# Optimization experiments

Hardware: AMD Instinct MI355X
Metric: run time of the kernel (lower is better)

The kernel has to match this reference:

```python
import jax, jax.numpy as jnp
import numpy as np

EPS = 1e-12
ALPHA = 100.0

def _l2norm(v, axis):
    n = jnp.sqrt(jnp.sum(v * v, axis=axis, keepdims=True))
    return v / jnp.maximum(n, EPS)

def setup_inputs() -> dict:
    key = jax.random.key(0)
    k1, k2, k3 = jax.random.split(key, 3)
    N, C, H, W, K = 64, 128, 64, 64, 64
    x = jax.random.normal(k1, (N, C, H, W), dtype=jnp.float32)
    xyz = jax.random.normal(k2, (N, 3, H * W), dtype=jnp.float32)
    centroids = jax.random.uniform(k3, (K, C), dtype=jnp.float32)
    # conv params are initialized from centroids as in _init_params
    conv_w = 2.0 * ALPHA * centroids              # [K, C] (1x1 kernel squeezed)
    conv_b = -ALPHA * jnp.linalg.norm(centroids, axis=1)  # [K]
    return {"x": x, "xyz": xyz, "centroids": centroids, "conv_w": conv_w, "conv_b": conv_b}

def reference(x, xyz, centroids, conv_w, conv_b):
    N, C = x.shape[:2]
    K = centroids.shape[0]
    # descriptor-wise L2 normalization over channel dim
    x = _l2norm(x, axis=1)
    xf = x.reshape(N, C, -1)                      # [N, C, P]
    # 1x1 conv == channel matmul; softmax over clusters
    logits = jnp.einsum('kc,ncp->nkp', conv_w, xf) + conv_b[None, :, None]
    a = jax.nn.softmax(logits, axis=1)            # [N, K, P]
    # vlad[n,k,c] = sum_p a*x  -  (sum_p a) * centroid  (algebraically equal to
    # the original broadcasted-residual construction, without the NKCP tensor)
    vlad = jnp.einsum('nkp,ncp->nkc', a, xf) - a.sum(axis=-1)[..., None] * centroids[None]
    vlad = _l2norm(vlad, axis=2)                  # intra-normalization
    vlad = vlad.reshape(N, -1)
    vlad = _l2norm(vlad, axis=1)
    return vlad[..., None]                        # [N, K*C, 1]
```

## Files before the change

kernel.cpp:

```cpp
#include <hip/hip_runtime.h>
#include <math.h>

#define N_ 64
#define C_ 128
#define K_ 64
#define P_ 4096
#define PT 32
#define TILES_PER_N 8
#define PB (P_ / TILES_PER_N)
#define NSUB (PB / PT)
#define XH_STR 132
#define XT_STR 36
#define AS_STR 66
#define RED_STR 33

typedef __attribute__((ext_vector_type(8))) short short8;
typedef __attribute__((ext_vector_type(4))) float f32x4;

union U4S8 { unsigned int u[4]; short8 s; };

__device__ __forceinline__ unsigned int pack_hl(float f) {
    unsigned int xb = __float_as_uint(f);
    float hif = __uint_as_float(xb & 0xffff0000u);
    float lo  = f - hif;
    unsigned int lob = __float_as_uint(lo) & 0xffff0000u;
    return (xb >> 16) | lob;
}

__device__ __forceinline__ void unpack8(const unsigned int p[8], short8& hi, short8& lo) {
    U4S8 h, l;
    #pragma unroll
    for (int j = 0; j < 4; ++j) {
        unsigned int a = p[2 * j], b = p[2 * j + 1];
        h.u[j] = (a & 0xffffu) | (b << 16);
        l.u[j] = (a >> 16) | (b & 0xffff0000u);
    }
    hi = h.s; lo = l.s;
}

#define MFMA16(a, b, c) __builtin_amdgcn_mfma_f32_16x16x32_bf16(a, b, c, 0, 0, 0)

__global__ __launch_bounds__(256, 3)
void netvlad_main(const float* __restrict__ x,
                  const float* __restrict__ conv_w,
                  const float* __restrict__ conv_b,
                  float* __restrict__ acc_part,
                  float* __restrict__ asum_part,
                  int use_atomic)
{
    __shared__ unsigned int xhat[PT * XH_STR];
    __shared__ unsigned int xT  [C_ * XT_STR];
    __shared__ unsigned int as_ [PT * AS_STR];
    __shared__ float        red [PT * RED_STR];
    __shared__ float        rn_ [PT];

    const int t  = threadIdx.x;
    const int wv = t >> 6;
    const int l  = t & 63;
    const int n    = blockIdx.x >> 3;
    const int tile = blockIdx.x & 7;

    const int mrow = l & 15;
    const int kq   = l >> 4;

    const int cq  = t >> 3;
    const int ppq = t & 7;

    const int scp   = 8 * wv + (l & 7);
    const int skseg = l >> 3;

    short8 whi[4], wlo[4];
    {
        const float* wrow = conv_w + (size_t)(16 * wv + mrow) * C_;
        #pragma unroll
        for (int s = 0; s < 4; ++s) {
            U4S8 h, lo_;
            #pragma unroll
            for (int j = 0; j < 4; ++j) {
                float f0 = wrow[s * 32 + kq * 8 + 2 * j];
                float f1 = wrow[s * 32 + kq * 8 + 2 * j + 1];
                unsigned int b0 = __float_as_uint(f0), b1 = __float_as_uint(f1);
                float l0 = f0 - __uint_as_float(b0 & 0xffff0000u);
                float l1 = f1 - __uint_as_float(b1 & 0xffff0000u);
                unsigned int lb0 = __float_as_uint(l0) >> 16;
                unsigned int lb1 = __float_as_uint(l1) >> 16;
                h.u[j]   = (b0 >> 16) | ((b1 >> 16) << 16);
                lo_.u[j] = lb0 | (lb1 << 16);
            }
            whi[s] = h.s; wlo[s] = lo_.s;
        }
    }

    float cb8[8];
    #pragma unroll
    for (int i = 0; i < 8; ++i) cb8[i] = conv_b[skseg * 8 + i];

    f32x4 accC[8];
    #pragma unroll
    for (int nt = 0; nt < 8; ++nt) accC[nt] = (f32x4){0.f, 0.f, 0.f, 0.f};
    float asum_acc[8];
    #pragma unroll
    for (int i = 0; i < 8; ++i) asum_acc[i] = 0.f;

    const float* xbase = x + ((size_t)n * C_) * P_ + tile * PB + 4 * ppq;

    float4 ld[4];
    #pragma unroll
    for (int cc = 0; cc < 4; ++cc)
        ld[cc] = *(const float4*)(xbase + (size_t)(4 * cq + cc) * P_);

    for (int sub = 0; sub < NSUB; ++sub) {
        __syncthreads();

        {
            unsigned int pk[4][4];
            float ssq[4] = {0.f, 0.f, 0.f, 0.f};
            #pragma unroll
            for (int cc = 0; cc < 4; ++cc) {
                const float* f = &ld[cc].x;
                #pragma unroll
                for (int j = 0; j < 4; ++j) {
                    pk[cc][j] = pack_hl(f[j]);
                    ssq[j] += f[j] * f[j];
                }
            }
            #pragma unroll
            for (int j = 0; j < 4; ++j) {
                uint4 v = make_uint4(pk[0][j], pk[1][j], pk[2][j], pk[3][j]);
                *(uint4*)(xhat + (4 * ppq + j) * XH_STR + 4 * cq) = v;
                red[(4 * ppq + j) * RED_STR + cq] = ssq[j];
            }
            #pragma unroll
            for (int cc = 0; cc < 4; ++cc) {
                uint4 v = make_uint4(pk[cc][0], pk[cc][1], pk[cc][2], pk[cc][3]);
                *(uint4*)(xT + (4 * cq + cc) * XT_STR + 4 * ppq) = v;
            }
        }
        if (sub + 1 < NSUB) {
            #pragma unroll
            for (int cc = 0; cc < 4; ++cc)
                ld[cc] = *(const float4*)(xbase + (size_t)(4 * cq + cc) * P_ + (sub + 1) * PT);
        }
        __syncthreads();

        if (t < PT) {
            float ss = 0.f;
            #pragma unroll
            for (int q = 0; q < 32; ++q) ss += red[t * RED_STR + q];
            rn_[t] = 1.f / fmaxf(sqrtf(ss), 1e-12f);
        }

        #pragma unroll
        for (int j = 0; j < 2; ++j) {
            f32x4 accA = (f32x4){0.f, 0.f, 0.f, 0.f};
            const unsigned int* rowp = xhat + (j * 16 + mrow) * XH_STR + kq * 8;
            #pragma unroll
            for (int s = 0; s < 4; ++s) {
                uint4 q0 = *(const uint4*)(rowp + s * 32);
                uint4 q1 = *(const uint4*)(rowp + s * 32 + 4);
                unsigned int p8[8] = {q0.x, q0.y, q0.z, q0.w, q1.x, q1.y, q1.z, q1.w};
                short8 bhi, blo;
                unpack8(p8, bhi, blo);
                accA = MFMA16(whi[s], bhi, accA);
                accA = MFMA16(whi[s], blo, accA);
                accA = MFMA16(wlo[s], bhi, accA);
                accA = MFMA16(wlo[s], blo, accA);
            }
            #pragma unroll
            for (int r = 0; r < 4; ++r)
                as_[(j * 16 + mrow) * AS_STR + 16 * wv + kq * 4 + r] =
                    __float_as_uint(accA[r]);
        }
        __syncthreads();

        {
            float rnv = rn_[scp];
            float lv[8];
            #pragma unroll
            for (int i = 0; i < 8; ++i)
                lv[i] = __uint_as_float(as_[scp * AS_STR + skseg * 8 + i]) * rnv + cb8[i];
            float m = lv[0];
            #pragma unroll
            for (int i = 1; i < 8; ++i) m = fmaxf(m, lv[i]);
            float s = 0.f;
            #pragma unroll
            for (int i = 0; i < 8; ++i) s += __expf(lv[i] - m);
            #pragma unroll
            for (int off = 8; off <= 32; off <<= 1) {
                float mo = __shfl_xor(m, off);
                float so = __shfl_xor(s, off);
                float Mn = fmaxf(m, mo);
                s = s * __expf(m - Mn) + so * __expf(mo - Mn);
                m = Mn;
            }
            float inv = 1.f / s;
            #pragma unroll
            for (int i = 0; i < 8; ++i) {
                float a = __expf(lv[i] - m) * inv;
                asum_acc[i] += a;
                as_[scp * AS_STR + skseg * 8 + i] = pack_hl(a * rnv);
            }
        }
        __syncthreads();

        {
            unsigned int pa[8];
            #pragma unroll
            for (int i = 0; i < 8; ++i)
                pa[i] = as_[(kq * 8 + i) * AS_STR + 16 * wv + mrow];
            short8 ahi, alo;
            unpack8(pa, ahi, alo);
            #pragma unroll
            for (int nt = 0; nt < 8; ++nt) {
                const unsigned int* rp = xT + (nt * 16 + mrow) * XT_STR + kq * 8;
                uint4 q0 = *(const uint4*)(rp);
                uint4 q1 = *(const uint4*)(rp + 4);
                unsigned int p8[8] = {q0.x, q0.y, q0.z, q0.w, q1.x, q1.y, q1.z, q1.w};
                short8 xhi, xlo;
                unpack8(p8, xhi, xlo);
                accC[nt] = MFMA16(ahi, xhi, accC[nt]);
                accC[nt] = MFMA16(ahi, xlo, accC[nt]);
                accC[nt] = MFMA16(alo, xhi, accC[nt]);
                accC[nt] = MFMA16(alo, xlo, accC[nt]);
            }
        }
    }

    __syncthreads();
    {
        #pragma unroll
        for (int i = 0; i < 8; ++i) {
            asum_acc[i] += __shfl_xor(asum_acc[i], 1);
            asum_acc[i] += __shfl_xor(asum_acc[i], 2);
            asum_acc[i] += __shfl_xor(asum_acc[i], 4);
        }
        float* fred = (float*)xhat;
        if ((l & 7) == 0) {
            #pragma unroll
            for (int i = 0; i < 8; ++i)
                fred[wv * 64 + skseg * 8 + i] = asum_acc[i];
        }
    }
    if (!use_atomic) {
        float* dst = acc_part + ((size_t)blockIdx.x * K_ + 16 * wv + kq * 4) * C_ + mrow;
        #pragma unroll
        for (int r = 0; r < 4; ++r)
            #pragma unroll
            for (int nt = 0; nt < 8; ++nt)
                dst[r * C_ + nt * 16] = accC[nt][r];
    } else {
        float* dst = acc_part + ((size_t)n * K_ + 16 * wv + kq * 4) * C_ + mrow;
        #pragma unroll
        for (int r = 0; r < 4; ++r)
            #pragma unroll
            for (int nt = 0; nt < 8; ++nt)
                atomicAdd(dst + r * C_ + nt * 16, accC[nt][r]);
    }
    __syncthreads();
    if (t < K_) {
        const float* fred = (const float*)xhat;
        float v = fred[0 * 64 + t] + fred[1 * 64 + t] + fred[2 * 64 + t] + fred[3 * 64 + t];
        if (use_atomic) atomicAdd(asum_part + n * K_ + t, v);
        else            asum_part[(size_t)blockIdx.x * K_ + t] = v;
    }
}

__global__ __launch_bounds__(256, 4)
void netvlad_finalize(const float* __restrict__ acc_part,
                      const float* __restrict__ asum_part,
                      const float* __restrict__ centroids,
                      float* __restrict__ out,
                      int npart)
{
    __shared__ float wred[4];
    const int t = threadIdx.x;
    const int n = blockIdx.x;
    const int k = t >> 2;
    const int part = t & 3;

    float a_k = 0.f;
    for (int s = 0; s < npart; ++s)
        a_k += asum_part[(size_t)(n * npart + s) * K_ + k];

    float4 vals[8];
    #pragma unroll
    for (int i = 0; i < 8; ++i) vals[i] = make_float4(0.f, 0.f, 0.f, 0.f);
    for (int s = 0; s < npart; ++s) {
        const float4* av = (const float4*)(acc_part
            + ((size_t)(n * npart + s) * K_ + k) * C_ + part * 32);
        #pragma unroll
        for (int i = 0; i < 8; ++i) {
            float4 a = av[i];
            vals[i].x += a.x; vals[i].y += a.y;
            vals[i].z += a.z; vals[i].w += a.w;
        }
    }

    const float4* cenv = (const float4*)(centroids + k * C_ + part * 32);
    float loc = 0.f;
    #pragma unroll
    for (int i = 0; i < 8; ++i) {
        float4 cv = cenv[i];
        float4 v = vals[i];
        v.x -= a_k * cv.x; v.y -= a_k * cv.y;
        v.z -= a_k * cv.z; v.w -= a_k * cv.w;
        vals[i] = v;
        loc += v.x * v.x + v.y * v.y + v.z * v.z + v.w * v.w;
    }
    loc += __shfl_xor(loc, 1);
    loc += __shfl_xor(loc, 2);
    float rk = 1.f / fmaxf(sqrtf(loc), 1e-12f);

    float tot = 0.f;
    #pragma unroll
    for (int i = 0; i < 8; ++i) {
        float4 v = vals[i];
        v.x *= rk; v.y *= rk; v.z *= rk; v.w *= rk;
        vals[i] = v;
        tot += v.x * v.x + v.y * v.y + v.z * v.z + v.w * v.w;
    }
    #pragma unroll
    for (int o = 1; o < 64; o <<= 1) tot += __shfl_xor(tot, o);
    if ((t & 63) == 0) wred[t >> 6] = tot;
    __syncthreads();
    float T = wred[0] + wred[1] + wred[2] + wred[3];
    float rtot = 1.f / fmaxf(sqrtf(T), 1e-12f);

    float4* outv = (float4*)(out + ((size_t)n * K_ + k) * C_ + part * 32);
    #pragma unroll
    for (int i = 0; i < 8; ++i) {
        float4 v = vals[i];
        v.x *= rtot; v.y *= rtot; v.z *= rtot; v.w *= rtot;
        outv[i] = v;
    }
}

extern "C" void kernel_launch(void* const* d_in, const int* in_sizes, int n_in,
                              void* d_out, int out_size, void* d_ws, size_t ws_size,
                              hipStream_t stream)
{
    const float* x      = (const float*)d_in[0];
    const float* cent   = (const float*)d_in[2];
    const float* conv_w = (const float*)d_in[3];
    const float* conv_b = (const float*)d_in[4];
    float* out = (float*)d_out;

    const int nblk = N_ * TILES_PER_N;
    size_t need = (size_t)nblk * K_ * C_ * sizeof(float)
                + (size_t)nblk * K_ * sizeof(float);
    int use_atomic = (ws_size >= need) ? 0 : 1;
    int npart = use_atomic ? 1 : TILES_PER_N;

    float* acc_part  = (float*)d_ws;
    float* asum_part = acc_part + (size_t)(use_atomic ? N_ : nblk) * K_ * C_;

    if (use_atomic) {
        size_t zbytes = ((size_t)N_ * K_ * C_ + (size_t)N_ * K_) * sizeof(float);
        hipMemsetAsync(d_ws, 0, zbytes, stream);
    }

    hipLaunchKernelGGL(netvlad_main, dim3(nblk), dim3(256), 0, stream,
                       x, conv_w, conv_b, acc_part, asum_part, use_atomic);
    hipLaunchKernelGGL(netvlad_finalize, dim3(N_), dim3(256), 0, stream,
                       acc_part, asum_part, cent, out, npart);
}
```

Before: 230.9 us.

## Split hi/lo bf16 planes in LDS with swizzle, drop lo*lo MFMA, retile waves

Stores x and the assignment matrix as separate pre-packed hi and lo bf16 planes in shared memory, using XOR-swizzled layouts, so MFMA operands load directly without unpack shuffles. The lo*lo MFMA term is dropped, leaving three MFMAs per product instead of four. The second GEMM is retiled so each wave owns 4x2 output tiles. The sum-of-squares reduction now uses cross-lane shuffles, and launch bounds drop to 2 blocks per SM. In exchange there is slightly lower precision, more LDS per block and possibly lower occupancy.

```diff
diff --git a/kernel.cpp b/kernel.cpp
--- a/kernel.cpp
+++ b/kernel.cpp
@@ -9,38 +9,24 @@
 #define TILES_PER_N 8
 #define PB (P_ / TILES_PER_N)
 #define NSUB (PB / PT)
-#define XH_STR 132
-#define XT_STR 36
-#define AS_STR 66
-#define RED_STR 33
 
 typedef __attribute__((ext_vector_type(8))) short short8;
 typedef __attribute__((ext_vector_type(4))) float f32x4;
 
-union U4S8 { unsigned int u[4]; short8 s; };
-
-__device__ __forceinline__ unsigned int pack_hl(float f) {
-    unsigned int xb = __float_as_uint(f);
-    float hif = __uint_as_float(xb & 0xffff0000u);
-    float lo  = f - hif;
-    unsigned int lob = __float_as_uint(lo) & 0xffff0000u;
-    return (xb >> 16) | lob;
-}
-
-__device__ __forceinline__ void unpack8(const unsigned int p[8], short8& hi, short8& lo) {
-    U4S8 h, l;
-    #pragma unroll
-    for (int j = 0; j < 4; ++j) {
-        unsigned int a = p[2 * j], b = p[2 * j + 1];
-        h.u[j] = (a & 0xffffu) | (b << 16);
-        l.u[j] = (a >> 16) | (b & 0xffff0000u);
-    }
-    hi = h.s; lo = l.s;
+union U4S8 { uint4 u4; unsigned int u[4]; short8 s; };
+
+__device__ __forceinline__ unsigned int pair_hi(float a, float b) {
+    return (__float_as_uint(b) & 0xffff0000u) | (__float_as_uint(a) >> 16);
+}
+__device__ __forceinline__ float lo_part(float f) {
+    return f - __uint_as_float(__float_as_uint(f) & 0xffff0000u);
 }
 
 #define MFMA16(a, b, c) __builtin_amdgcn_mfma_f32_16x16x32_bf16(a, b, c, 0, 0, 0)
 
-__global__ __launch_bounds__(256, 3)
+__device__ __forceinline__ int pmask(int p) { return (p & 7) ^ ((p >> 3) & 3); }
+
+__global__ __launch_bounds__(256, 2)
 void netvlad_main(const float* __restrict__ x,
                   const float* __restrict__ conv_w,
                   const float* __restrict__ conv_b,
@@ -48,10 +34,14 @@
                   float* __restrict__ asum_part,
                   int use_atomic)
 {
-    __shared__ unsigned int xhat[PT * XH_STR];
-    __shared__ unsigned int xT  [C_ * XT_STR];
-    __shared__ unsigned int as_ [PT * AS_STR];
-    __shared__ float        red [PT * RED_STR];
+    __shared__ unsigned int xhi [PT * 64];
+    __shared__ unsigned int xlo [PT * 64];
+    __shared__ unsigned int xthi[C_ * 20];
+    __shared__ unsigned int xtlo[C_ * 20];
+    __shared__ unsigned int ahi_[K_ * 20];
+    __shared__ unsigned int alo_[K_ * 20];
+    __shared__ float        asl [PT * 68];
+    __shared__ float        red2[4 * 33];
     __shared__ float        rn_ [PT];
 
     const int t  = threadIdx.x;
@@ -63,122 +53,140 @@
     const int mrow = l & 15;
     const int kq   = l >> 4;
 
+    const int ppq = t & 7;
     const int cq  = t >> 3;
-    const int ppq = t & 7;
-
-    const int scp   = 8 * wv + (l & 7);
-    const int skseg = l >> 3;
-
-    short8 whi[4], wlo[4];
-    {
-        const float* wrow = conv_w + (size_t)(16 * wv + mrow) * C_;
+
+    const int kseg = l >> 3;
+    const int scol = 8 * wv + (l & 7);
+
+    const int ntp = wv & 1;
+    const int mt0 = 2 * (wv >> 1);
+
+    short8 whi[2][4], wlo[2][4];
+    #pragma unroll
+    for (int mtl = 0; mtl < 2; ++mtl) {
+        const float* wr = conv_w + (size_t)((mt0 + mtl) * 16 + mrow) * C_;
         #pragma unroll
         for (int s = 0; s < 4; ++s) {
-            U4S8 h, lo_;
+            U4S8 h, lo;
             #pragma unroll
             for (int j = 0; j < 4; ++j) {
-                float f0 = wrow[s * 32 + kq * 8 + 2 * j];
-                float f1 = wrow[s * 32 + kq * 8 + 2 * j + 1];
-                unsigned int b0 = __float_as_uint(f0), b1 = __float_as_uint(f1);
-                float l0 = f0 - __uint_as_float(b0 & 0xffff0000u);
-                float l1 = f1 - __uint_as_float(b1 & 0xffff0000u);
-                unsigned int lb0 = __float_as_uint(l0) >> 16;
-                unsigned int lb1 = __float_as_uint(l1) >> 16;
-                h.u[j]   = (b0 >> 16) | ((b1 >> 16) << 16);
-                lo_.u[j] = lb0 | (lb1 << 16);
-            }
-            whi[s] = h.s; wlo[s] = lo_.s;
-        }
-    }
-
+                float f0 = wr[s * 32 + kq * 8 + 2 * j];
+                float f1 = wr[s * 32 + kq * 8 + 2 * j + 1];
+                h.u[j]  = pair_hi(f0, f1);
+                lo.u[j] = pair_hi(lo_part(f0), lo_part(f1));
+            }
+            whi[mtl][s] = h.s; wlo[mtl][s] = lo.s;
+        }
+    }
     float cb8[8];
     #pragma unroll
-    for (int i = 0; i < 8; ++i) cb8[i] = conv_b[skseg * 8 + i];
-
-    f32x4 accC[8];
-    #pragma unroll
-    for (int nt = 0; nt < 8; ++nt) accC[nt] = (f32x4){0.f, 0.f, 0.f, 0.f};
+    for (int i = 0; i < 8; ++i) cb8[i] = conv_b[kseg * 8 + i];
+
+    f32x4 accC[4][2];
+    #pragma unroll
+    for (int mt = 0; mt < 4; ++mt)
+        #pragma unroll
+        for (int ntl = 0; ntl < 2; ++ntl) accC[mt][ntl] = (f32x4){0.f, 0.f, 0.f, 0.f};
     float asum_acc[8];
     #pragma unroll
     for (int i = 0; i < 8; ++i) asum_acc[i] = 0.f;
 
-    const float* xbase = x + ((size_t)n * C_) * P_ + tile * PB + 4 * ppq;
+    const float* xb = x + ((size_t)n * C_) * P_ + tile * PB + 4 * ppq;
 
     float4 ld[4];
     #pragma unroll
     for (int cc = 0; cc < 4; ++cc)
-        ld[cc] = *(const float4*)(xbase + (size_t)(4 * cq + cc) * P_);
+        ld[cc] = *(const float4*)(xb + (size_t)(4 * cq + cc) * P_);
 
     for (int sub = 0; sub < NSUB; ++sub) {
         __syncthreads();
 
         {
-            unsigned int pk[4][4];
-            float ssq[4] = {0.f, 0.f, 0.f, 0.f};
+            const float* lf = (const float*)ld;
             #pragma unroll
             for (int cc = 0; cc < 4; ++cc) {
-                const float* f = &ld[cc].x;
+                float4 v = ld[cc];
+                int c = 4 * cq + cc;
+                uint2 wh; wh.x = pair_hi(v.x, v.y); wh.y = pair_hi(v.z, v.w);
+                *(uint2*)(xthi + c * 20 + 2 * ppq) = wh;
+                uint2 wl; wl.x = pair_hi(lo_part(v.x), lo_part(v.y));
+                wl.y = pair_hi(lo_part(v.z), lo_part(v.w));
+                *(uint2*)(xtlo + c * 20 + 2 * ppq) = wl;
+            }
+            float ssq[4];
+            #pragma unroll
+            for (int j = 0; j < 4; ++j) {
+                int p = 4 * ppq + j;
+                int ch = cq >> 1;
+                int chp = (ch & 8) | ((ch ^ pmask(p)) & 7);
+                int base = p * 64 + (chp << 2) + ((cq & 1) << 1);
+                float f0 = lf[0 * 4 + j], f1 = lf[1 * 4 + j];
+                float f2 = lf[2 * 4 + j], f3 = lf[3 * 4 + j];
+                uint2 wh; wh.x = pair_hi(f0, f1); wh.y = pair_hi(f2, f3);
+                *(uint2*)(xhi + base) = wh;
+                uint2 wl; wl.x = pair_hi(lo_part(f0), lo_part(f1));
+                wl.y = pair_hi(lo_part(f2), lo_part(f3));
+                *(uint2*)(xlo + base) = wl;
+                ssq[j] = f0 * f0 + f1 * f1 + f2 * f2 + f3 * f3;
+            }
+            #pragma unroll
+            for (int j = 0; j < 4; ++j) {
+                ssq[j] += __shfl_xor(ssq[j], 8);
+                ssq[j] += __shfl_xor(ssq[j], 16);
+                ssq[j] += __shfl_xor(ssq[j], 32);
+            }
+            if (l < 8) {
                 #pragma unroll
-                for (int j = 0; j < 4; ++j) {
-                    pk[cc][j] = pack_hl(f[j]);
-                    ssq[j] += f[j] * f[j];
-                }
-            }
-            #pragma unroll
-            for (int j = 0; j < 4; ++j) {
-                uint4 v = make_uint4(pk[0][j], pk[1][j], pk[2][j], pk[3][j]);
-                *(uint4*)(xhat + (4 * ppq + j) * XH_STR + 4 * cq) = v;
-                red[(4 * ppq + j) * RED_STR + cq] = ssq[j];
-            }
-            #pragma unroll
-            for (int cc = 0; cc < 4; ++cc) {
-                uint4 v = make_uint4(pk[cc][0], pk[cc][1], pk[cc][2], pk[cc][3]);
-                *(uint4*)(xT + (4 * cq + cc) * XT_STR + 4 * ppq) = v;
+                for (int j = 0; j < 4; ++j) red2[wv * 33 + 4 * l + j] = ssq[j];
             }
         }
         if (sub + 1 < NSUB) {
             #pragma unroll
             for (int cc = 0; cc < 4; ++cc)
-                ld[cc] = *(const float4*)(xbase + (size_t)(4 * cq + cc) * P_ + (sub + 1) * PT);
+                ld[cc] = *(const float4*)(xb + (size_t)(4 * cq + cc) * P_ + (sub + 1) * PT);
         }
         __syncthreads();
 
         if (t < PT) {
-            float ss = 0.f;
-            #pragma unroll
-            for (int q = 0; q < 32; ++q) ss += red[t * RED_STR + q];
+            float ss = red2[t] + red2[33 + t] + red2[66 + t] + red2[99 + t];
             rn_[t] = 1.f / fmaxf(sqrtf(ss), 1e-12f);
         }
 
-        #pragma unroll
-        for (int j = 0; j < 2; ++j) {
-            f32x4 accA = (f32x4){0.f, 0.f, 0.f, 0.f};
-            const unsigned int* rowp = xhat + (j * 16 + mrow) * XH_STR + kq * 8;
+        {
+            const int prow = ntp * 16 + mrow;
+            const int msk = pmask(prow);
+            f32x4 a0 = (f32x4){0.f, 0.f, 0.f, 0.f};
+            f32x4 a1 = (f32x4){0.f, 0.f, 0.f, 0.f};
             #pragma unroll
             for (int s = 0; s < 4; ++s) {
-                uint4 q0 = *(const uint4*)(rowp + s * 32);
-                uint4 q1 = *(const uint4*)(rowp + s * 32 + 4);
-                unsigned int p8[8] = {q0.x, q0.y, q0.z, q0.w, q1.x, q1.y, q1.z, q1.w};
-                short8 bhi, blo;
-                unpack8(p8, bhi, blo);
-                accA = MFMA16(whi[s], bhi, accA);
-                accA = MFMA16(whi[s], blo, accA);
-                accA = MFMA16(wlo[s], bhi, accA);
-                accA = MFMA16(wlo[s], blo, accA);
-            }
-            #pragma unroll
-            for (int r = 0; r < 4; ++r)
-                as_[(j * 16 + mrow) * AS_STR + 16 * wv + kq * 4 + r] =
-                    __float_as_uint(accA[r]);
+                int ch = s * 4 + kq;
+                int chp = (ch & 8) | ((ch ^ msk) & 7);
+                int idx = prow * 64 + (chp << 2);
+                U4S8 bh, bl;
+                bh.u4 = *(const uint4*)(xhi + idx);
+                bl.u4 = *(const uint4*)(xlo + idx);
+                a0 = MFMA16(whi[0][s], bh.s, a0);
+                a0 = MFMA16(whi[0][s], bl.s, a0);
+                a0 = MFMA16(wlo[0][s], bh.s, a0);
+                a1 = MFMA16(whi[1][s], bh.s, a1);
+                a1 = MFMA16(whi[1][s], bl.s, a1);
+                a1 = MFMA16(wlo[1][s], bh.s, a1);
+            }
+            *(f32x4*)(asl + prow * 68 + (mt0    ) * 16 + kq * 4) = a0;
+            *(f32x4*)(asl + prow * 68 + (mt0 + 1) * 16 + kq * 4) = a1;
         }
         __syncthreads();
 
         {
-            float rnv = rn_[scp];
+            float rnv = rn_[scol];
+            f32x4 q0 = *(const f32x4*)(asl + scol * 68 + kseg * 8);
+            f32x4 q1 = *(const f32x4*)(asl + scol * 68 + kseg * 8 + 4);
             float lv[8];
             #pragma unroll
-            for (int i = 0; i < 8; ++i)
-                lv[i] = __uint_as_float(as_[scp * AS_STR + skseg * 8 + i]) * rnv + cb8[i];
+            for (int i = 0; i < 4; ++i) { lv[i] = q0[i] * rnv + cb8[i]; }
+            #pragma unroll
+            for (int i = 0; i < 4; ++i) { lv[4 + i] = q1[i] * rnv + cb8[4 + i]; }
             float m = lv[0];
             #pragma unroll
             for (int i = 1; i < 8; ++i) m = fmaxf(m, lv[i]);
@@ -194,72 +202,87 @@
                 m = Mn;
             }
             float inv = 1.f / s;
+            const int p2 = scol >> 1;
             #pragma unroll
             for (int i = 0; i < 8; ++i) {
                 float a = __expf(lv[i] - m) * inv;
                 asum_acc[i] += a;
-                as_[scp * AS_STR + skseg * 8 + i] = pack_hl(a * rnv);
+                float av = a * rnv;
+                float pav = __shfl_xor(av, 1);
+                if ((l & 1) == 0) {
+                    int k = kseg * 8 + i;
+                    int chp = wv ^ (kseg & 3);
+                    int off = k * 20 + (chp << 2) + (p2 & 3);
+                    ahi_[off] = pair_hi(av, pav);
+                    alo_[off] = pair_hi(lo_part(av), lo_part(pav));
+                }
             }
         }
         __syncthreads();
 
         {
-            unsigned int pa[8];
-            #pragma unroll
-            for (int i = 0; i < 8; ++i)
-                pa[i] = as_[(kq * 8 + i) * AS_STR + 16 * wv + mrow];
-            short8 ahi, alo;
-            unpack8(pa, ahi, alo);
-            #pragma unroll
-            for (int nt = 0; nt < 8; ++nt) {
-                const unsigned int* rp = xT + (nt * 16 + mrow) * XT_STR + kq * 8;
-                uint4 q0 = *(const uint4*)(rp);
-                uint4 q1 = *(const uint4*)(rp + 4);
-                unsigned int p8[8] = {q0.x, q0.y, q0.z, q0.w, q1.x, q1.y, q1.z, q1.w};
-                short8 xhi, xlo;
-                unpack8(p8, xhi, xlo);
-                accC[nt] = MFMA16(ahi, xhi, accC[nt]);
-                accC[nt] = MFMA16(ahi, xlo, accC[nt]);
-                accC[nt] = MFMA16(alo, xhi, accC[nt]);
-                accC[nt] = MFMA16(alo, xlo, accC[nt]);
+            U4S8 ah[4], al[4];
+            #pragma unroll
+            for (int mt = 0; mt < 4; ++mt) {
+                int ar = mt * 16 + mrow;
+                int chp = kq ^ ((ar >> 3) & 3);
+                int idx = ar * 20 + (chp << 2);
+                ah[mt].u4 = *(const uint4*)(ahi_ + idx);
+                al[mt].u4 = *(const uint4*)(alo_ + idx);
+            }
+            #pragma unroll
+            for (int ntl = 0; ntl < 2; ++ntl) {
+                int cr = (2 * wv + ntl) * 16 + mrow;
+                int xi = cr * 20 + kq * 4;
+                U4S8 xh, xl2;
+                xh.u4  = *(const uint4*)(xthi + xi);
+                xl2.u4 = *(const uint4*)(xtlo + xi);
+                #pragma unroll
+                for (int mt = 0; mt < 4; ++mt) {
+                    accC[mt][ntl] = MFMA16(ah[mt].s, xh.s,  accC[mt][ntl]);
+                    accC[mt][ntl] = MFMA16(ah[mt].s, xl2.s, accC[mt][ntl]);
+                    accC[mt][ntl] = MFMA16(al[mt].s, xh.s,  accC[mt][ntl]);
+                }
             }
         }
     }
 
     __syncthreads();
-    {
-        #pragma unroll
-        for (int i = 0; i < 8; ++i) {
-            asum_acc[i] += __shfl_xor(asum_acc[i], 1);
-            asum_acc[i] += __shfl_xor(asum_acc[i], 2);
-            asum_acc[i] += __shfl_xor(asum_acc[i], 4);
-        }
-        float* fred = (float*)xhat;
-        if ((l & 7) == 0) {
-            #pragma unroll
-            for (int i = 0; i < 8; ++i)
-                fred[wv * 64 + skseg * 8 + i] = asum_acc[i];
-        }
+    #pragma unroll
+    for (int i = 0; i < 8; ++i) {
+        asum_acc[i] += __shfl_xor(asum_acc[i], 1);
+        asum_acc[i] += __shfl_xor(asum_acc[i], 2);
+        asum_acc[i] += __shfl_xor(asum_acc[i], 4);
+    }
+    float* fred = (float*)xhi;
+    if ((l & 7) == 0) {
+        #pragma unroll
+        for (int i = 0; i < 8; ++i) fred[wv * 64 + kseg * 8 + i] = asum_acc[i];
     }
     if (!use_atomic) {
-        float* dst = acc_part + ((size_t)blockIdx.x * K_ + 16 * wv + kq * 4) * C_ + mrow;
-        #pragma unroll
-        for (int r = 0; r < 4; ++r)
-            #pragma unroll
-            for (int nt = 0; nt < 8; ++nt)
-                dst[r * C_ + nt * 16] = accC[nt][r];
+        float* dst = acc_part + (size_t)blockIdx.x * K_ * C_;
+        #pragma unroll
+        for (int mt = 0; mt < 4; ++mt)
+            #pragma unroll
+            for (int r = 0; r < 4; ++r)
+                #pragma unroll
+                for (int ntl = 0; ntl < 2; ++ntl)
+                    dst[(mt * 16 + kq * 4 + r) * C_ + (2 * wv + ntl) * 16 + mrow] =
+                        accC[mt][ntl][r];
     } else {
-        float* dst = acc_part + ((size_t)n * K_ + 16 * wv + kq * 4) * C_ + mrow;
-        #pragma unroll
-        for (int r = 0; r < 4; ++r)
-            #pragma unroll
-            for (int nt = 0; nt < 8; ++nt)
-                atomicAdd(dst + r * C_ + nt * 16, accC[nt][r]);
+        float* dst = acc_part + (size_t)n * K_ * C_;
+        #pragma unroll
+        for (int mt = 0; mt < 4; ++mt)
+            #pragma unroll
+            for (int r = 0; r < 4; ++r)
+                #pragma unroll
+                for (int ntl = 0; ntl < 2; ++ntl)
+                    atomicAdd(dst + (mt * 16 + kq * 4 + r) * C_ + (2 * wv + ntl) * 16 + mrow,
+                              accC[mt][ntl][r]);
     }
     __syncthreads();
     if (t < K_) {
-        const float* fred = (const float*)xhat;
-        float v = fred[0 * 64 + t] + fred[1 * 64 + t] + fred[2 * 64 + t] + fred[3 * 64 + t];
+        float v = fred[t] + fred[64 + t] + fred[128 + t] + fred[192 + t];
         if (use_atomic) atomicAdd(asum_part + n * K_ + t, v);
         else            asum_part[(size_t)blockIdx.x * K_ + t] = v;
     }
```

After: 222.1 us. 3.8% less time.
